# Optimization experiments

Hardware: AMD Instinct MI355X
Metric: run time of the kernel (lower is better)

The kernel has to match this reference:

```python
import jax, jax.numpy as jnp
import numpy as np
from jax import lax

TAU = 2.0        # LIFNode default tau, decay_input=True, v_reset=0.0
V_TH = 1.0       # default threshold
SG_ALPHA = 4.0   # surrogate.Sigmoid default alpha
EPS = 1e-5


@jax.custom_vjp
def spike_fn(v):
    return (v >= V_TH).astype(v.dtype)

def _spike_fwd(v):
    return spike_fn(v), v

def _spike_bwd(v, g):
    sg = jax.nn.sigmoid(SG_ALPHA * (v - V_TH))
    return (g * SG_ALPHA * sg * (1.0 - sg),)

spike_fn.defvjp(_spike_fwd, _spike_bwd)


def lif(x_seq):
    """Multi-step LIF: x_seq [T, ...] -> spikes [T, ...]. Hard reset to 0."""
    def step(v, x):
        v = v + (x - v) / TAU          # decay_input integration, v_reset=0
        s = spike_fn(v)
        v = v * (1.0 - s)              # hard reset
        return v, s
    v0 = jnp.zeros_like(x_seq[0])
    _, s_seq = lax.scan(step, v0, x_seq)
    return s_seq


def conv3x3(x, w):
    # x [N,C,H,W], w [O,I,3,3], padding=1, no bias
    return lax.conv_general_dilated(x, w, (1, 1), ((1, 1), (1, 1)),
                                    dimension_numbers=('NCHW', 'OIHW', 'NCHW'))


def tdbn(x, gamma, beta):
    # ThresholdDependentBatchNorm2d: BN over merged (T*B, H, W) per channel
    m = x.mean(axis=(0, 2, 3), keepdims=True)
    v = x.var(axis=(0, 2, 3), keepdims=True)
    return (x - m) * lax.rsqrt(v + EPS) * gamma[None, :, None, None] + beta[None, :, None, None]


def maxpool2(x):
    return lax.reduce_window(x, -jnp.inf, lax.max, (1, 1, 2, 2), (1, 1, 2, 2), 'VALID')


def setup_inputs() -> dict:
    key = jax.random.key(0)
    ks = jax.random.split(key, 5)
    T, B, H, W = 16, 32, 32, 400
    x = jax.random.normal(ks[0], (T, B, 1, H, W), dtype=jnp.float32)
    w1 = jax.random.normal(ks[1], (6, 1, 3, 3), dtype=jnp.float32) * (1.0 / 3.0)
    w2 = jax.random.normal(ks[2], (6, 6, 3, 3), dtype=jnp.float32) * (1.0 / jnp.sqrt(54.0))
    w3 = jax.random.normal(ks[3], (6, 6, 3, 3), dtype=jnp.float32) * (1.0 / jnp.sqrt(54.0))
    kf = jax.random.split(ks[4], 2)
    fw1 = jax.random.normal(kf[0], (100, 1200), dtype=jnp.float32) * (1.0 / jnp.sqrt(1200.0))
    fw2 = jax.random.normal(kf[1], (2, 100), dtype=jnp.float32) * (1.0 / 10.0)
    ones6 = jnp.ones((6,), jnp.float32)
    zeros6 = jnp.zeros((6,), jnp.float32)
    return {"x": x, "w1": w1, "g1": ones6, "b1": zeros6,
            "w2": w2, "g2": ones6, "b2": zeros6,
            "w3": w3, "g3": ones6, "b3": zeros6,
            "fw1": fw1, "fw2": fw2}


def _forward(x, w1, g1, b1, w2, g2, b2, w3, g3, b3, fw1, fw2):
    T, B = x.shape[0], x.shape[1]

    def block(s_seq, w, g, b):
        # conv + tdBN + LIF + maxpool over [T,B,C,H,W]
        TB = s_seq.reshape((T * B,) + s_seq.shape[2:])
        y = tdbn(conv3x3(TB, w), g, b)
        y = y.reshape((T, B) + y.shape[1:])
        s = lif(y)
        p = maxpool2(s.reshape((T * B,) + s.shape[2:]))
        return p.reshape((T, B) + p.shape[1:])

    h = block(x, w1, g1, b1)
    h = block(h, w2, g2, b2)
    h = block(h, w3, g3, b3)          # [T, B, 6, 4, 50]

    h = h.reshape(T, B, -1)            # flatten (C,H,W) -> 1200
    h = lif(jnp.einsum('tbf,of->tbo', h, fw1))   # [T, B, 100]
    out = lif(jnp.einsum('tbf,of->tbo', h, fw2)) # [T, B, 2]
    return out


def reference(x, w1, g1, b1, w2, g2, b2, w3, g3, b3, fw1, fw2):
    return _forward(x, w1, g1, b1, w2, g2, b2, w3, g3, b3, fw1, fw2)
```

## Files before the change

### kernel.cpp

```cpp
#include <hip/hip_runtime.h>


namespace {

constexpr int T = 16, B = 32;
constexpr int H1 = 32, W1 = 400, P1H = 16, P1W = 200;
constexpr int H2 = 16, W2 = 200, P2H = 8,  P2W = 100;
constexpr int H3 = 8,  W3 = 100, P3H = 4,  P3W = 50;

constexpr int NWG_S1 = T * B * (H1 / 32) * (W1 / 100);
constexpr int NWG_F1 = B * (P1H / 4) * (P1W / 10);
constexpr int NWG_F2 = B * (P2H / 4) * (P2W / 5);

constexpr size_t OFF_PART1  = 0;
constexpr size_t OFF_PARTF1 = OFF_PART1 + (size_t)NWG_S1 * 12 * 8;
constexpr size_t OFF_PARTF2 = OFF_PARTF1 + (size_t)6400 * 12 * 8;
constexpr size_t OFF_STATS  = OFF_PARTF2 + (size_t)2560 * 12 * 8;
constexpr size_t OFF_POOL1  = 1310720;
constexpr size_t OFF_POOL2  = OFF_POOL1 + (size_t)T * B * 6 * P1H * P1W * 4;
constexpr size_t OFF_POOL3  = OFF_POOL2 + (size_t)T * B * 6 * P2H * P2W * 4;
constexpr size_t OFF_U1     = OFF_POOL3 + (size_t)T * B * 6 * P3H * P3W * 4;

}

#define LDS_PHASE_BARRIER()                                   \
  do {                                                        \
    asm volatile("s_waitcnt lgkmcnt(0)" ::: "memory");        \
    __builtin_amdgcn_s_barrier();                             \
    __builtin_amdgcn_sched_barrier(0);                        \
  } while (0)

__device__ __forceinline__ float lif_step(float& v, float y) {
  v = v + (y - v) * 0.5f;
  float sp = (v >= 1.0f) ? 1.0f : 0.0f;
  v = (sp > 0.0f) ? 0.0f : v;
  return sp;
}

__device__ __forceinline__ void reduce12(double* s, double* q, double* partials) {
  __shared__ double lds[4][12];
  int lane = threadIdx.x & 63, wid = threadIdx.x >> 6;
#pragma unroll
  for (int k = 0; k < 12; k++) {
    double v = (k < 6) ? s[k] : q[k - 6];
#pragma unroll
    for (int off = 32; off >= 1; off >>= 1) v += __shfl_down(v, off, 64);
    if (lane == 0) lds[wid][k] = v;
  }
  __syncthreads();
  if (threadIdx.x < 12) {
    partials[(size_t)blockIdx.x * 12 + threadIdx.x] =
        lds[0][threadIdx.x] + lds[1][threadIdx.x] + lds[2][threadIdx.x] + lds[3][threadIdx.x];
  }
}

__device__ __forceinline__ void reduce12_sel(int oidx, double s_acc, double q_acc,
                                             double* partials) {
  __shared__ double lds[4][12];
  int lane = threadIdx.x & 63, wid = threadIdx.x >> 6;
#pragma unroll
  for (int k = 0; k < 12; k++) {
    double v = (k == oidx) ? s_acc : ((k == oidx + 6) ? q_acc : 0.0);
#pragma unroll
    for (int off = 32; off >= 1; off >>= 1) v += __shfl_down(v, off, 64);
    if (lane == 0) lds[wid][k] = v;
  }
  __syncthreads();
  if (threadIdx.x < 12) {
    partials[(size_t)blockIdx.x * 12 + threadIdx.x] =
        lds[0][threadIdx.x] + lds[1][threadIdx.x] + lds[2][threadIdx.x] + lds[3][threadIdx.x];
  }
}

template <int NC, int H, int W, int TH, int TW>
__global__ void conv_stats_lds(const float* __restrict__ in, const float* __restrict__ wt,
                               double* __restrict__ partials) {
  constexpr int IH = TH + 2, IW = TW + 2;
  constexpr int IWP = (IW & 1) ? IW : IW + 1;
  constexpr int NW = NC * 54;
  constexpr int NTH = H / TH, NTW = W / TW;
  constexpr int NT = NTH * NTW;
  __shared__ float wsm[NW];
  __shared__ float tile[NC][IH][IWP];

  int tid = threadIdx.x;
  for (int k = tid; k < NW; k += blockDim.x) wsm[k] = wt[k];

  int wg = blockIdx.x;
  int tb = wg / NT;
  int ti = wg % NT;
  int ty = ti / NTW, tx = ti % NTW;
  int h0 = ty * TH - 1, w0 = tx * TW - 1;
  const float* xb = in + (size_t)tb * NC * H * W;

  for (int k = tid; k < NC * IH * IW; k += blockDim.x) {
    int i = k / (IH * IW);
    int r = k % (IH * IW);
    int rr = r / IW, cc = r % IW;
    int hh = h0 + rr, ww = w0 + cc;
    tile[i][rr][cc] = (hh >= 0 && hh < H && ww >= 0 && ww < W) ? xb[i * H * W + hh * W + ww] : 0.0f;
  }
  __syncthreads();

  double s[6] = {0, 0, 0, 0, 0, 0}, q[6] = {0, 0, 0, 0, 0, 0};
  for (int pos = tid; pos < TH * TW; pos += blockDim.x) {
    int ly = pos / TW, lx = pos % TW;
    float acc[6] = {0, 0, 0, 0, 0, 0};
#pragma unroll
    for (int i = 0; i < NC; i++) {
      float p[9];
#pragma unroll
      for (int ky = 0; ky < 3; ky++)
#pragma unroll
        for (int kx = 0; kx < 3; kx++) p[ky * 3 + kx] = tile[i][ly + ky][lx + kx];
#pragma unroll
      for (int o = 0; o < 6; o++) {
        float a = acc[o];
#pragma unroll
        for (int k2 = 0; k2 < 9; k2++) a = fmaf(p[k2], wsm[(o * NC + i) * 9 + k2], a);
        acc[o] = a;
      }
    }
#pragma unroll
    for (int o = 0; o < 6; o++) {
      s[o] += (double)acc[o];
      q[o] += (double)acc[o] * (double)acc[o];
    }
  }
  reduce12(s, q, partials);
}

__global__ void finalize_stats(const double* __restrict__ partials, int nb, double n,
                               const float* __restrict__ gamma,
                               float* __restrict__ mean_out, float* __restrict__ sg_out) {
  __shared__ double lds[12][21];
  __shared__ double sums[12];
  int t = threadIdx.x;
  int k = t % 12, j = t / 12;
  if (t < 252) {
    double acc = 0.0;
    for (int b = j; b < nb; b += 21) acc += partials[(size_t)b * 12 + k];
    lds[k][j] = acc;
  }
  __syncthreads();
  if (t < 12) {
    double acc = 0.0;
#pragma unroll
    for (int j2 = 0; j2 < 21; j2++) acc += lds[t][j2];
    sums[t] = acc;
  }
  __syncthreads();
  if (t < 6) {
    double mean = sums[t] / n;
    double var = sums[t + 6] / n - mean * mean;
    double invstd = 1.0 / sqrt(var + 1e-5);
    mean_out[t] = (float)mean;
    sg_out[t] = (float)(invstd * (double)gamma[t]);
  }
}

__global__ void fuse1_stats(const float* __restrict__ x, const float* __restrict__ w1g,
                            const float* __restrict__ w2g,
                            const float* __restrict__ mean1, const float* __restrict__ sg1,
                            const float* __restrict__ beta1,
                            float* __restrict__ pool1, double* __restrict__ partials2) {
  __shared__ float wsm1[54];
  __shared__ float wsm2[324];
  __shared__ float til[2][14][13];
  __shared__ float phl[432];
  __shared__ float pr[40][7][7];

  int tid = threadIdx.x;
  for (int k = tid; k < 54; k += 256) wsm1[k] = w1g[k];
  for (int k = tid; k < 324; k += 256) wsm2[k] = w2g[k];

  int wg = blockIdx.x;
  int b = wg / 80;
  int rem = wg % 80;
  int oy = rem / 20, ox = rem % 20;
  int iy0 = 8 * oy - 3, ix0 = 20 * ox - 3;

  bool s_in[2];
  int s_off[2], s_lofs[2];
#pragma unroll
  for (int j = 0; j < 2; j++) {
    int k = tid + 256 * j;
    bool valid = k < 364;
    int srr = k / 26, scc = k % 26;
    int shh = iy0 + srr, sww = ix0 + scc;
    s_in[j] = valid && shh >= 0 && shh < H1 && sww >= 0 && sww < W1;
    s_off[j] = shh * W1 + sww;
    s_lofs[j] = valid ? ((scc & 1) * 182 + srr * 13 + (scc >> 1)) : -1;
  }
  float* tilf = &til[0][0][0];

  int hch[2], hhy[2], hhx[2], hpy[2], hpx[2];
  bool hact[2], hval[2], hown[2];
  float m_[2], sc_[2], be_[2];
  float wv[2][9];
#pragma unroll
  for (int sl = 0; sl < 2; sl++) {
    int pos = tid + 256 * sl;
    hact[sl] = pos < 432;
    int p2 = hact[sl] ? pos : 0;
    int ch = p2 / 72;
    int r = p2 % 72;
    int hy = r / 12, hx = r % 12;
    hch[sl] = ch; hhy[sl] = hy; hhx[sl] = hx;
    int py = 4 * oy - 1 + hy, px = 10 * ox - 1 + hx;
    hpy[sl] = py; hpx[sl] = px;
    hval[sl] = hact[sl] && py >= 0 && py < P1H && px >= 0 && px < P1W;
    hown[sl] = hact[sl] && hy >= 1 && hy <= 4 && hx >= 1 && hx <= 10;
#pragma unroll
    for (int k = 0; k < 9; k++) wv[sl][k] = w1g[ch * 9 + k];
    m_[sl] = mean1[ch]; sc_[sl] = sg1[ch]; be_[sl] = beta1[ch];
  }

  int oidx = (tid < 240) ? (tid / 40) : -1;
  int pos40 = tid % 40;
  int psy = pos40 / 10, psx = pos40 % 10;

  float v[2][4];
#pragma unroll
  for (int sl = 0; sl < 2; sl++)
#pragma unroll
    for (int k = 0; k < 4; k++) v[sl][k] = 0.0f;
  double s_acc = 0.0, q_acc = 0.0;

  float rs[2] = {0.0f, 0.0f};
#pragma unroll
  for (int j = 0; j < 2; j++)
    if (s_in[j]) rs[j] = x[(size_t)(0 * B + b) * (H1 * W1) + s_off[j]];

  for (int t = 0; t < T; t++) {
    __syncthreads();
#pragma unroll
    for (int j = 0; j < 2; j++)
      if (s_lofs[j] >= 0) tilf[s_lofs[j]] = rs[j];
    if (t + 1 < T) {
#pragma unroll
      for (int j = 0; j < 2; j++)
        if (s_in[j]) rs[j] = x[(size_t)((t + 1) * B + b) * (H1 * W1) + s_off[j]];
    }
    LDS_PHASE_BARRIER();
#pragma unroll
    for (int sl = 0; sl < 2; sl++) {
      if (hact[sl]) {
        float smax = 0.0f;
        if (hval[sl]) {
          int ry = 2 * hhy[sl], hx = hhx[sl];
          float p[16];
#pragma unroll
          for (int r = 0; r < 4; r++) {
            p[r * 4 + 0] = til[0][ry + r][hx];
            p[r * 4 + 1] = til[1][ry + r][hx];
            p[r * 4 + 2] = til[0][ry + r][hx + 1];
            p[r * 4 + 3] = til[1][ry + r][hx + 1];
          }
#pragma unroll
          for (int dy = 0; dy < 2; dy++) {
#pragma unroll
            for (int dx = 0; dx < 2; dx++) {
              float acc = 0.0f;
#pragma unroll
              for (int ky = 0; ky < 3; ky++)
#pragma unroll
                for (int kx = 0; kx < 3; kx++)
                  acc = fmaf(p[(dy + ky) * 4 + dx + kx], wv[sl][ky * 3 + kx], acc);
              float y = (acc - m_[sl]) * sc_[sl] + be_[sl];
              float sp = lif_step(v[sl][dy * 2 + dx], y);
              smax = fmaxf(smax, sp);
            }
          }
        }
        phl[tid + 256 * sl] = smax;
        if (hown[sl])
          pool1[((size_t)(t * B + b) * 6 + hch[sl]) * (P1H * P1W) + hpy[sl] * P1W + hpx[sl]] = smax;
      }
    }
    LDS_PHASE_BARRIER();
    if (oidx >= 0) {
      int i2 = oidx;
      float pt[9];
#pragma unroll
      for (int ky = 0; ky < 3; ky++)
#pragma unroll
        for (int kx = 0; kx < 3; kx++)
          pt[ky * 3 + kx] = phl[i2 * 72 + (psy + ky) * 12 + (psx + kx)];
      float p6[6];
#pragma unroll
      for (int o = 0; o < 6; o++) {
        float a = 0.0f;
#pragma unroll
        for (int k2 = 0; k2 < 9; k2++) a = fmaf(pt[k2], wsm2[(o * 6 + i2) * 9 + k2], a);
        p6[o] = a;
      }
#pragma unroll
      for (int o = 0; o < 6; o++) pr[pos40][i2][o] = p6[o];
    }
    LDS_PHASE_BARRIER();
    if (oidx >= 0) {
      double acc = 0.0;
#pragma unroll
      for (int ic = 0; ic < 6; ic++) acc += (double)pr[pos40][ic][oidx];
      s_acc += acc;
      q_acc += acc * acc;
    }
  }
  __syncthreads();
  reduce12_sel(oidx, s_acc, q_acc, partials2);
}

__global__ void fuse2_stats(const float* __restrict__ in, const float* __restrict__ w2g,
                            const float* __restrict__ w3g,
                            const float* __restrict__ mean2, const float* __restrict__ sg2,
                            const float* __restrict__ beta2,
                            float* __restrict__ pool2, double* __restrict__ partials3) {
  __shared__ float wsm2[324];
  __shared__ float wsm3[324];
  __shared__ float til[2][6][14][9];
  __shared__ float phl[6][6][7];
  __shared__ float pr[20][6][7];

  int tid = threadIdx.x;
  for (int k = tid; k < 324; k += 256) { wsm2[k] = w2g[k]; wsm3[k] = w3g[k]; }

  int wg = blockIdx.x;
  int b = wg / 40;
  int rem = wg % 40;
  int oy = rem / 20, ox = rem % 20;
  int iy0 = 8 * oy - 3, ix0 = 10 * ox - 3;
  constexpr int HW = H2 * W2;

  bool s_in[6];
  int s_off[6], s_lofs[6];
#pragma unroll
  for (int j = 0; j < 6; j++) {
    int k = tid + 256 * j;
    bool valid = k < 1344;
    int i = k / 224;
    int r2 = k % 224;
    int rr = r2 / 16, cc = r2 % 16;
    int hh = iy0 + rr, ww = ix0 + cc;
    s_in[j] = valid && hh >= 0 && hh < H2 && ww >= 0 && ww < W2;
    s_off[j] = i * HW + hh * W2 + ww;
    s_lofs[j] = valid ? ((cc & 1) * 756 + i * 126 + rr * 9 + (cc >> 1)) : -1;
  }
  float* tilf = &til[0][0][0][0];

  bool active = tid < 252;
  int ch = 0, hy = 0, hx = 0, py = 0, px = 0;
  bool pvalid = false, own = false;
  if (active) {
    ch = tid / 42;
    int r = tid % 42;
    hy = r / 7; hx = r % 7;
    py = 4 * oy - 1 + hy; px = 5 * ox - 1 + hx;
    pvalid = (py >= 0 && py < P2H && px >= 0 && px < P2W);
    own = (hy >= 1 && hy <= 4 && hx >= 1 && hx <= 5);
  }
  float m = active ? mean2[ch] : 0.0f;
  float sc = active ? sg2[ch] : 0.0f;
  float be = active ? beta2[ch] : 0.0f;

  int oidx = (tid < 120) ? (tid / 20) : -1;
  int pos = tid % 20;
  int psy = pos / 5, psx = pos % 5;

  float v[4] = {0.0f, 0.0f, 0.0f, 0.0f};
  double s_acc = 0.0, q_acc = 0.0;

  float rs[6] = {0.0f, 0.0f, 0.0f, 0.0f, 0.0f, 0.0f};
  {
    const float* xb = in + (size_t)(0 * B + b) * 6 * HW;
#pragma unroll
    for (int j = 0; j < 6; j++)
      if (s_in[j]) rs[j] = xb[s_off[j]];
  }

  for (int t = 0; t < T; t++) {
    __syncthreads();
#pragma unroll
    for (int j = 0; j < 6; j++)
      if (s_lofs[j] >= 0) tilf[s_lofs[j]] = rs[j];
    if (t + 1 < T) {
      const float* xb = in + (size_t)((t + 1) * B + b) * 6 * HW;
#pragma unroll
      for (int j = 0; j < 6; j++)
        if (s_in[j]) rs[j] = xb[s_off[j]];
    }
    LDS_PHASE_BARRIER();
    if (active) {
      float smax = 0.0f;
      if (pvalid) {
        int ry = 2 * hy;
        float acc4[4] = {0.0f, 0.0f, 0.0f, 0.0f};
#pragma unroll
        for (int i = 0; i < 6; i++) {
          float p[16];
#pragma unroll
          for (int r = 0; r < 4; r++) {
            p[r * 4 + 0] = til[0][i][ry + r][hx];
            p[r * 4 + 1] = til[1][i][ry + r][hx];
            p[r * 4 + 2] = til[0][i][ry + r][hx + 1];
            p[r * 4 + 3] = til[1][i][ry + r][hx + 1];
          }
          const float* wo = &wsm2[(ch * 6 + i) * 9];
#pragma unroll
          for (int dy = 0; dy < 2; dy++)
#pragma unroll
            for (int dx = 0; dx < 2; dx++) {
              float a = acc4[dy * 2 + dx];
#pragma unroll
              for (int ky = 0; ky < 3; ky++)
#pragma unroll
                for (int kx = 0; kx < 3; kx++)
                  a = fmaf(p[(dy + ky) * 4 + dx + kx], wo[ky * 3 + kx], a);
              acc4[dy * 2 + dx] = a;
            }
        }
#pragma unroll
        for (int p4 = 0; p4 < 4; p4++) {
          float y = (acc4[p4] - m) * sc + be;
          float sp = lif_step(v[p4], y);
          smax = fmaxf(smax, sp);
        }
      }
      phl[ch][hy][hx] = smax;
      if (own)
        pool2[((size_t)(t * B + b) * 6 + ch) * (P2H * P2W) + py * P2W + px] = smax;
    }
    LDS_PHASE_BARRIER();
    if (oidx >= 0) {
      float pt[9];
#pragma unroll
      for (int ky = 0; ky < 3; ky++)
#pragma unroll
        for (int kx = 0; kx < 3; kx++)
          pt[ky * 3 + kx] = phl[oidx][psy + ky][psx + kx];
      float p6[6];
#pragma unroll
      for (int o = 0; o < 6; o++) {
        float a = 0.0f;
#pragma unroll
        for (int k2 = 0; k2 < 9; k2++) a = fmaf(pt[k2], wsm3[(o * 6 + oidx) * 9 + k2], a);
        p6[o] = a;
      }
#pragma unroll
      for (int o = 0; o < 6; o++) pr[pos][oidx][o] = p6[o];
    }
    LDS_PHASE_BARRIER();
    if (oidx >= 0) {
      double acc = 0.0;
#pragma unroll
      for (int ic = 0; ic < 6; ic++) acc += (double)pr[pos][ic][oidx];
      s_acc += acc;
      q_acc += acc * acc;
    }
  }
  __syncthreads();
  reduce12_sel(oidx, s_acc, q_acc, partials3);
}

template <int H, int W, int PH, int PW, int TH, int TW>
__global__ void block6_fuse_lds(const float* __restrict__ in, const float* __restrict__ wt,
                                const float* __restrict__ mean, const float* __restrict__ sg,
                                const float* __restrict__ beta, float* __restrict__ out) {
  constexpr int NTH = PH / TH, NTW = PW / TW;
  constexpr int IH = 2 * TH + 2, IW = 2 * TW + 2;
  constexpr int EW = IW / 2;
  constexpr int TILE_N = IH * IW;
  constexpr int NACT = 6 * TH * TW;
  constexpr int HW = H * W;
  __shared__ float wsm[324];
  __shared__ float til_e[6][IH][EW];
  __shared__ float til_o[6][IH][EW];

  for (int k = threadIdx.x; k < 324; k += blockDim.x) wsm[k] = wt[k];

  int wg = blockIdx.x;
  int b = wg / (NTH * NTW);
  int tid2 = wg % (NTH * NTW);
  int ty = tid2 / NTW, tx = tid2 % NTW;
  int h_in0 = 2 * (ty * TH) - 1, w_in0 = 2 * (tx * TW) - 1;

  int tid = threadIdx.x;
  int o = 0, lph = 0, lpw = 0;
  if (tid < NACT) {
    o = tid / (TH * TW);
    int r = tid % (TH * TW);
    lph = r / TW; lpw = r % TW;
  }
  float m = mean[o], s = sg[o], be = beta[o];
  float v[4] = {0.0f, 0.0f, 0.0f, 0.0f};

  for (int t = 0; t < T; t++) {
    __syncthreads();
    const float* xb = in + (size_t)(t * B + b) * 6 * HW;
    for (int k = tid; k < 6 * TILE_N; k += blockDim.x) {
      int i = k / TILE_N;
      int r2 = k % TILE_N;
      int rr = r2 / IW, cc = r2 % IW;
      int hh = h_in0 + rr, ww = w_in0 + cc;
      float val = (hh >= 0 && hh < H && ww >= 0 && ww < W) ? xb[i * HW + hh * W + ww] : 0.0f;
      if (cc & 1) til_o[i][rr][cc >> 1] = val;
      else        til_e[i][rr][cc >> 1] = val;
    }
    __syncthreads();
    if (tid < NACT) {
      int ry = 2 * lph;
      float acc[4] = {0.0f, 0.0f, 0.0f, 0.0f};
#pragma unroll
      for (int i = 0; i < 6; i++) {
        float p[16];
#pragma unroll
        for (int r = 0; r < 4; r++) {
          p[r * 4 + 0] = til_e[i][ry + r][lpw];
          p[r * 4 + 1] = til_o[i][ry + r][lpw];
          p[r * 4 + 2] = til_e[i][ry + r][lpw + 1];
          p[r * 4 + 3] = til_o[i][ry + r][lpw + 1];
        }
        const float* wo = &wsm[(o * 6 + i) * 9];
#pragma unroll
        for (int dy = 0; dy < 2; dy++)
#pragma unroll
          for (int dx = 0; dx < 2; dx++) {
            float a = acc[dy * 2 + dx];
#pragma unroll
            for (int ky = 0; ky < 3; ky++)
#pragma unroll
              for (int kx = 0; kx < 3; kx++)
                a = fmaf(p[(dy + ky) * 4 + dx + kx], wo[ky * 3 + kx], a);
            acc[dy * 2 + dx] = a;
          }
      }
      float smax = 0.0f;
#pragma unroll
      for (int p4 = 0; p4 < 4; p4++) {
        float y = (acc[p4] - m) * s + be;
        float sp = lif_step(v[p4], y);
        smax = fmaxf(smax, sp);
      }
      out[((size_t)(t * B + b) * 6 + o) * (PH * PW) + (ty * TH + lph) * PW + (tx * TW + lpw)] = smax;
    }
  }
}

__global__ void fc1_mm(const float* __restrict__ p3, const float* __restrict__ fw1,
                       float* __restrict__ u1) {
  int idx = blockIdx.x * blockDim.x + threadIdx.x;
  if (idx >= T * B * 100) return;
  int o = idx % 100;
  int tb = idx / 100;
  const float4* x4 = (const float4*)(p3 + (size_t)tb * 1200);
  const float4* w4 = (const float4*)(fw1 + (size_t)o * 1200);
  float acc = 0.0f;
#pragma unroll 4
  for (int k = 0; k < 300; k++) {
    float4 a = x4[k], w = w4[k];
    acc = fmaf(a.x, w.x, acc);
    acc = fmaf(a.y, w.y, acc);
    acc = fmaf(a.z, w.z, acc);
    acc = fmaf(a.w, w.w, acc);
  }
  u1[idx] = acc;
}

__global__ void fc_tail(const float* __restrict__ u1, const float* __restrict__ fw2,
                        float* __restrict__ outp) {
  __shared__ float s1[100];
  __shared__ float w2s[200];
  int b = blockIdx.x;
  int tid = threadIdx.x;
  for (int k = tid; k < 200; k += 128) w2s[k] = fw2[k];
  float v1 = 0.0f, v2 = 0.0f;
  __syncthreads();
  for (int t = 0; t < T; t++) {
    if (tid < 100) {
      float sp = lif_step(v1, u1[(size_t)(t * B + b) * 100 + tid]);
      s1[tid] = sp;
    }
    __syncthreads();
    if (tid < 2) {
      const float* wr = &w2s[tid * 100];
      float acc = 0.0f;
#pragma unroll
      for (int k = 0; k < 100; k++) acc = fmaf(s1[k], wr[k], acc);
      float sp = lif_step(v2, acc);
      outp[(size_t)(t * B + b) * 2 + tid] = sp;
    }
    __syncthreads();
  }
}

extern "C" void kernel_launch(void* const* d_in, const int* in_sizes, int n_in,
                              void* d_out, int out_size, void* d_ws, size_t ws_size,
                              hipStream_t stream) {
  const float* x   = (const float*)d_in[0];
  const float* w1  = (const float*)d_in[1];
  const float* g1  = (const float*)d_in[2];
  const float* b1  = (const float*)d_in[3];
  const float* w2  = (const float*)d_in[4];
  const float* g2  = (const float*)d_in[5];
  const float* b2  = (const float*)d_in[6];
  const float* w3  = (const float*)d_in[7];
  const float* g3  = (const float*)d_in[8];
  const float* b3  = (const float*)d_in[9];
  const float* fw1 = (const float*)d_in[10];
  const float* fw2 = (const float*)d_in[11];
  float* out = (float*)d_out;

  char* ws = (char*)d_ws;
  double* part1  = (double*)(ws + OFF_PART1);
  double* partf1 = (double*)(ws + OFF_PARTF1);
  double* partf2 = (double*)(ws + OFF_PARTF2);
  float* mean1 = (float*)(ws + OFF_STATS + 0);
  float* sg1   = (float*)(ws + OFF_STATS + 32);
  float* mean2 = (float*)(ws + OFF_STATS + 64);
  float* sg2   = (float*)(ws + OFF_STATS + 96);
  float* mean3 = (float*)(ws + OFF_STATS + 128);
  float* sg3   = (float*)(ws + OFF_STATS + 160);
  float* pool1 = (float*)(ws + OFF_POOL1);
  float* pool2 = (float*)(ws + OFF_POOL2);
  float* pool3 = (float*)(ws + OFF_POOL3);
  float* u1    = (float*)(ws + OFF_U1);

  conv_stats_lds<1, H1, W1, 32, 100><<<NWG_S1, 256, 0, stream>>>(x, w1, part1);
  finalize_stats<<<1, 256, 0, stream>>>(part1, NWG_S1, (double)T * B * H1 * W1, g1, mean1, sg1);
  fuse1_stats<<<NWG_F1, 256, 0, stream>>>(x, w1, w2, mean1, sg1, b1, pool1, partf1);
  finalize_stats<<<1, 256, 0, stream>>>(partf1, NWG_F1, (double)T * B * H2 * W2, g2, mean2, sg2);
  fuse2_stats<<<NWG_F2, 256, 0, stream>>>(pool1, w2, w3, mean2, sg2, b2, pool2, partf2);
  finalize_stats<<<1, 256, 0, stream>>>(partf2, NWG_F2, (double)T * B * H3 * W3, g3, mean3, sg3);
  {
    int nwg = B * (P3H / 2) * (P3W / 5);
    block6_fuse_lds<H3, W3, P3H, P3W, 2, 5><<<nwg, 64, 0, stream>>>(pool2, w3, mean3, sg3, b3, pool3);
  }
  {
    int n = T * B * 100;
    fc1_mm<<<(n + 255) / 256, 256, 0, stream>>>(pool3, fw1, u1);
  }
  fc_tail<<<B, 128, 0, stream>>>(u1, fw2, out);
}
```

Before: 433.1 us.

## Enlarge fuse2_stats tile to full pooled height per workgroup

```diff
diff --git a/kernel.cpp b/kernel.cpp
--- a/kernel.cpp
+++ b/kernel.cpp
@@ -10,7 +10,7 @@
 
 constexpr int NWG_S1 = T * B * (H1 / 32) * (W1 / 100);
 constexpr int NWG_F1 = B * (P1H / 4) * (P1W / 10);
-constexpr int NWG_F2 = B * (P2H / 4) * (P2W / 5);
+constexpr int NWG_F2 = B * (P2W / 5);
 
 constexpr size_t OFF_PART1  = 0;
 constexpr size_t OFF_PARTF1 = OFF_PART1 + (size_t)NWG_S1 * 12 * 8;
@@ -318,142 +318,154 @@
                             float* __restrict__ pool2, double* __restrict__ partials3) {
   __shared__ float wsm2[324];
   __shared__ float wsm3[324];
-  __shared__ float til[2][6][14][9];
-  __shared__ float phl[6][6][7];
-  __shared__ float pr[20][6][7];
+  __shared__ float til[2][6][22][9];
+  __shared__ float phl[420];
+  __shared__ float pr[40][7][7];
 
   int tid = threadIdx.x;
   for (int k = tid; k < 324; k += 256) { wsm2[k] = w2g[k]; wsm3[k] = w3g[k]; }
 
   int wg = blockIdx.x;
-  int b = wg / 40;
-  int rem = wg % 40;
-  int oy = rem / 20, ox = rem % 20;
-  int iy0 = 8 * oy - 3, ix0 = 10 * ox - 3;
+  int b = wg / 20;
+  int ox = wg % 20;
+  int ix0 = 10 * ox - 3;
   constexpr int HW = H2 * W2;
 
-  bool s_in[6];
-  int s_off[6], s_lofs[6];
-#pragma unroll
-  for (int j = 0; j < 6; j++) {
+  int s_off[9], s_lofs[9];
+#pragma unroll
+  for (int j = 0; j < 9; j++) {
     int k = tid + 256 * j;
-    bool valid = k < 1344;
-    int i = k / 224;
-    int r2 = k % 224;
+    bool valid = k < 2112;
+    int i = k / 352;
+    int r2 = k % 352;
     int rr = r2 / 16, cc = r2 % 16;
-    int hh = iy0 + rr, ww = ix0 + cc;
-    s_in[j] = valid && hh >= 0 && hh < H2 && ww >= 0 && ww < W2;
-    s_off[j] = i * HW + hh * W2 + ww;
-    s_lofs[j] = valid ? ((cc & 1) * 756 + i * 126 + rr * 9 + (cc >> 1)) : -1;
+    int hh = -3 + rr, ww = ix0 + cc;
+    bool in_b = valid && hh >= 0 && hh < H2 && ww >= 0 && ww < W2;
+    s_off[j] = in_b ? (i * HW + hh * W2 + ww) : -1;
+    s_lofs[j] = valid ? ((cc & 1) * 1188 + i * 198 + rr * 9 + (cc >> 1)) : -1;
   }
   float* tilf = &til[0][0][0][0];
 
-  bool active = tid < 252;
-  int ch = 0, hy = 0, hx = 0, py = 0, px = 0;
-  bool pvalid = false, own = false;
-  if (active) {
-    ch = tid / 42;
-    int r = tid % 42;
-    hy = r / 7; hx = r % 7;
-    py = 4 * oy - 1 + hy; px = 5 * ox - 1 + hx;
-    pvalid = (py >= 0 && py < P2H && px >= 0 && px < P2W);
-    own = (hy >= 1 && hy <= 4 && hx >= 1 && hx <= 5);
-  }
-  float m = active ? mean2[ch] : 0.0f;
-  float sc = active ? sg2[ch] : 0.0f;
-  float be = active ? beta2[ch] : 0.0f;
-
-  int oidx = (tid < 120) ? (tid / 20) : -1;
-  int pos = tid % 20;
-  int psy = pos / 5, psx = pos % 5;
-
-  float v[4] = {0.0f, 0.0f, 0.0f, 0.0f};
+  int hch[2], hhy[2], hhx[2], hpy[2], hpx[2];
+  bool hact[2], hval[2], hown[2];
+  float m_[2], sc_[2], be_[2];
+#pragma unroll
+  for (int sl = 0; sl < 2; sl++) {
+    int pos = tid + 256 * sl;
+    hact[sl] = pos < 420;
+    int p2 = hact[sl] ? pos : 0;
+    int ch = p2 / 70;
+    int r = p2 % 70;
+    int hy = r / 7, hx = r % 7;
+    hch[sl] = ch; hhy[sl] = hy; hhx[sl] = hx;
+    int py = hy - 1, px = 5 * ox - 1 + hx;
+    hpy[sl] = py; hpx[sl] = px;
+    hval[sl] = hact[sl] && py >= 0 && py < P2H && px >= 0 && px < P2W;
+    hown[sl] = hact[sl] && hy >= 1 && hy <= 8 && hx >= 1 && hx <= 5;
+    m_[sl] = mean2[ch]; sc_[sl] = sg2[ch]; be_[sl] = beta2[ch];
+  }
+
+  int oidx = (tid < 240) ? (tid / 40) : -1;
+  int pos40 = tid % 40;
+  int psy = pos40 / 5, psx = pos40 % 5;
+
+  float v[2][4];
+#pragma unroll
+  for (int sl = 0; sl < 2; sl++)
+#pragma unroll
+    for (int k = 0; k < 4; k++) v[sl][k] = 0.0f;
   double s_acc = 0.0, q_acc = 0.0;
 
-  float rs[6] = {0.0f, 0.0f, 0.0f, 0.0f, 0.0f, 0.0f};
+  float rs[9];
+#pragma unroll
+  for (int j = 0; j < 9; j++) rs[j] = 0.0f;
   {
     const float* xb = in + (size_t)(0 * B + b) * 6 * HW;
 #pragma unroll
-    for (int j = 0; j < 6; j++)
-      if (s_in[j]) rs[j] = xb[s_off[j]];
+    for (int j = 0; j < 9; j++)
+      if (s_off[j] >= 0) rs[j] = xb[s_off[j]];
   }
 
   for (int t = 0; t < T; t++) {
     __syncthreads();
 #pragma unroll
-    for (int j = 0; j < 6; j++)
+    for (int j = 0; j < 9; j++)
       if (s_lofs[j] >= 0) tilf[s_lofs[j]] = rs[j];
     if (t + 1 < T) {
       const float* xb = in + (size_t)((t + 1) * B + b) * 6 * HW;
 #pragma unroll
-      for (int j = 0; j < 6; j++)
-        if (s_in[j]) rs[j] = xb[s_off[j]];
+      for (int j = 0; j < 9; j++)
+        if (s_off[j] >= 0) rs[j] = xb[s_off[j]];
     }
     LDS_PHASE_BARRIER();
-    if (active) {
-      float smax = 0.0f;
-      if (pvalid) {
-        int ry = 2 * hy;
-        float acc4[4] = {0.0f, 0.0f, 0.0f, 0.0f};
-#pragma unroll
-        for (int i = 0; i < 6; i++) {
-          float p[16];
-#pragma unroll
-          for (int r = 0; r < 4; r++) {
-            p[r * 4 + 0] = til[0][i][ry + r][hx];
-            p[r * 4 + 1] = til[1][i][ry + r][hx];
-            p[r * 4 + 2] = til[0][i][ry + r][hx + 1];
-            p[r * 4 + 3] = til[1][i][ry + r][hx + 1];
+#pragma unroll
+    for (int sl = 0; sl < 2; sl++) {
+      if (hact[sl]) {
+        float smax = 0.0f;
+        if (hval[sl]) {
+          int ry = 2 * hhy[sl], hx = hhx[sl], ch = hch[sl];
+          float acc4[4] = {0.0f, 0.0f, 0.0f, 0.0f};
+#pragma unroll
+          for (int i = 0; i < 6; i++) {
+            float p[16];
+#pragma unroll
+            for (int r = 0; r < 4; r++) {
+              p[r * 4 + 0] = til[0][i][ry + r][hx];
+              p[r * 4 + 1] = til[1][i][ry + r][hx];
+              p[r * 4 + 2] = til[0][i][ry + r][hx + 1];
+              p[r * 4 + 3] = til[1][i][ry + r][hx + 1];
+            }
+            const float* wo = &wsm2[(ch * 6 + i) * 9];
+#pragma unroll
+            for (int dy = 0; dy < 2; dy++)
+#pragma unroll
+              for (int dx = 0; dx < 2; dx++) {
+                float a = acc4[dy * 2 + dx];
+#pragma unroll
+                for (int ky = 0; ky < 3; ky++)
+#pragma unroll
+                  for (int kx = 0; kx < 3; kx++)
+                    a = fmaf(p[(dy + ky) * 4 + dx + kx], wo[ky * 3 + kx], a);
+                acc4[dy * 2 + dx] = a;
+              }
           }
-          const float* wo = &wsm2[(ch * 6 + i) * 9];
-#pragma unroll
-          for (int dy = 0; dy < 2; dy++)
-#pragma unroll
-            for (int dx = 0; dx < 2; dx++) {
-              float a = acc4[dy * 2 + dx];
-#pragma unroll
-              for (int ky = 0; ky < 3; ky++)
-#pragma unroll
-                for (int kx = 0; kx < 3; kx++)
-                  a = fmaf(p[(dy + ky) * 4 + dx + kx], wo[ky * 3 + kx], a);
-              acc4[dy * 2 + dx] = a;
-            }
+#pragma unroll
+          for (int p4 = 0; p4 < 4; p4++) {
+            float y = (acc4[p4] - m_[sl]) * sc_[sl] + be_[sl];
+            float sp = lif_step(v[sl][p4], y);
+            smax = fmaxf(smax, sp);
+          }
         }
-#pragma unroll
-        for (int p4 = 0; p4 < 4; p4++) {
-          float y = (acc4[p4] - m) * sc + be;
-          float sp = lif_step(v[p4], y);
-          smax = fmaxf(smax, sp);
-        }
+        phl[tid + 256 * sl] = smax;
+        if (hown[sl])
+          pool2[((size_t)(t * B + b) * 6 + hch[sl]) * (P2H * P2W) + hpy[sl] * P2W + hpx[sl]] = smax;
       }
-      phl[ch][hy][hx] = smax;
-      if (own)
-        pool2[((size_t)(t * B + b) * 6 + ch) * (P2H * P2W) + py * P2W + px] = smax;
     }
     LDS_PHASE_BARRIER();
     if (oidx >= 0) {
+      int i2 = oidx;
       float pt[9];
 #pragma unroll
       for (int ky = 0; ky < 3; ky++)
 #pragma unroll
         for (int kx = 0; kx < 3; kx++)
-          pt[ky * 3 + kx] = phl[oidx][psy + ky][psx + kx];
+          pt[ky * 3 + kx] = phl[i2 * 70 + (psy + ky) * 7 + (psx + kx)];
       float p6[6];
 #pragma unroll
       for (int o = 0; o < 6; o++) {
         float a = 0.0f;
 #pragma unroll
-        for (int k2 = 0; k2 < 9; k2++) a = fmaf(pt[k2], wsm3[(o * 6 + oidx) * 9 + k2], a);
+        for (int k2 = 0; k2 < 9; k2++) a = fmaf(pt[k2], wsm3[(o * 6 + i2) * 9 + k2], a);
         p6[o] = a;
       }
 #pragma unroll
-      for (int o = 0; o < 6; o++) pr[pos][oidx][o] = p6[o];
+      for (int o = 0; o < 6; o++) pr[pos40][i2][o] = p6[o];
     }
     LDS_PHASE_BARRIER();
     if (oidx >= 0) {
       double acc = 0.0;
 #pragma unroll
-      for (int ic = 0; ic < 6; ic++) acc += (double)pr[pos][ic][oidx];
+      for (int ic = 0; ic < 6; ic++) acc += (double)pr[pos40][ic][oidx];
       s_acc += acc;
       q_acc += acc * acc;
     }
```

New measurement: 510.9 us. +18.0%, slower.
